# Kernel optimization log

Hardware: AMD Instinct MI355X
Metric: run time of the kernel (lower is better)

## Reference

```python
import jax, jax.numpy as jnp
import numpy as np

N, D_IN, E, H, F, T = 50000, 128, 800000, 8, 32, 8
NEG_SLOPE = 0.2


def setup_inputs() -> dict:
    key = jax.random.key(0)
    ks = jax.random.split(key, 12)
    feat = jax.random.normal(ks[0], (N, D_IN), dtype=jnp.float32)
    edge_embeddings = jax.random.normal(ks[1], (E, H), dtype=jnp.float32)
    src = jax.random.randint(ks[2], (E,), 0, N, dtype=jnp.int32)
    dst = jnp.sort(jax.random.randint(ks[3], (E,), 0, N, dtype=jnp.int32))
    etype = jax.random.randint(ks[4], (E,), 0, T, dtype=jnp.int32)
    s = 0.05
    W_src = jax.random.normal(ks[5], (H * F, D_IN), dtype=jnp.float32) * s
    attn_l = jax.random.normal(ks[6], (1, H, F), dtype=jnp.float32) * s
    attn_r = jax.random.normal(ks[7], (1, H, F), dtype=jnp.float32) * s
    attn_e = jax.random.normal(ks[8], (1, H, F), dtype=jnp.float32) * s
    W_e = jax.random.normal(ks[9], (H * F, H), dtype=jnp.float32) * s
    type_emb = jax.random.normal(ks[10], (T, F), dtype=jnp.float32) * s
    k2 = jax.random.split(ks[11], 3)
    W_et = jax.random.normal(k2[0], (H * F, F), dtype=jnp.float32) * s
    attn_et = jax.random.normal(k2[1], (1, H, F), dtype=jnp.float32) * s
    bias = jnp.zeros((H * F,), dtype=jnp.float32)
    return dict(feat=feat, edge_embeddings=edge_embeddings, src=src, dst=dst,
                etype=etype, W_src=W_src, attn_l=attn_l, attn_r=attn_r,
                attn_e=attn_e, W_e=W_e, type_emb=type_emb, W_et=W_et,
                attn_et=attn_et, bias=bias)


def _leaky_relu(x):
    return jnp.where(x >= 0, x, NEG_SLOPE * x)


def reference(feat, edge_embeddings, src, dst, etype, W_src, attn_l, attn_r,
              attn_e, W_e, type_emb, W_et, attn_et, bias):
    n = feat.shape[0]
    # node transform (shared src/dst weights)
    fs = (feat @ W_src.T).reshape(n, H, F)           # [N,H,F]
    el = (fs * attn_l).sum(-1)                        # [N,H]
    er = (fs * attn_r).sum(-1)                        # [N,H]
    e = el[src] + er[dst]                             # [E,H] (u_add_v)
    # edge embedding attention term
    ee = (edge_embeddings @ W_e.T).reshape(-1, H, F)  # [E,H,F]
    e_score = (ee * attn_e).sum(-1)                   # [E,H]
    # edge type embedding attention term
    te = type_emb[etype]                              # [E,F]
    te = (te @ W_et.T).reshape(-1, H, F)              # [E,H,F]
    t_score = (te * attn_et).sum(-1)                  # [E,H]
    attn = e + e_score + t_score                      # attn_agg = sum
    # edge-type frequency normalization
    counts = jnp.bincount(etype, length=T).astype(jnp.float32)
    w = counts.sum() / (T * counts)                   # [T]
    attn = attn * w[etype][:, None]
    attn = _leaky_relu(attn)                          # v2=False -> after agg
    # edge softmax over incoming edges of each dst node
    m = jax.ops.segment_max(attn, dst, num_segments=n)  # [N,H]
    a = jnp.exp(attn - m[dst])
    z = jax.ops.segment_sum(a, dst, num_segments=n)     # [N,H]
    a = a / z[dst]                                      # [E,H]
    # weighted scatter aggregation
    msg = fs[src] * a[:, :, None]                       # [E,H,F]
    out = jax.ops.segment_sum(msg, dst, num_segments=n) # [N,H,F]
    return out + bias.reshape(1, H, F)
```

## Files before the change

### kernel.cpp

```cpp
#include <hip/hip_runtime.h>
#include <math.h>

#define N_NODES 50000
#define D_IN    128
#define E_EDGES 800000
#define H_HEADS 8
#define F_FEAT  32
#define T_TYPES 8
#define HF      256
#define NEG_SLOPE 0.2f
#define HIST_BLOCKS 256
#define GEMM_BLOCKS 208
#define OFF_BLOCKS  196
#define K1_HIST_BASE GEMM_BLOCKS
#define K1_OFF_BASE  (GEMM_BLOCKS + HIST_BLOCKS)
#define K1_GRID      (GEMM_BLOCKS + HIST_BLOCKS + OFF_BLOCKS)
#define NGROUPS      ((N_NODES + 63) / 64)

using short8 = __attribute__((__ext_vector_type__(8))) short;
using f32x4  = __attribute__((__ext_vector_type__(4))) float;

__device__ inline float bf2f(unsigned short u) {
    union { unsigned int i; float f; } v; v.i = ((unsigned int)u) << 16; return v.f;
}
__device__ inline unsigned short f2bf(float f) {
    unsigned int x = __float_as_uint(f);
    unsigned int r = (x + 0x7fffu + ((x >> 16) & 1u)) >> 16;
    return (unsigned short)r;
}
__device__ inline unsigned int pk2bf(float a, float b) {
    return (unsigned int)f2bf(a) | ((unsigned int)f2bf(b) << 16);
}

__global__ __launch_bounds__(256) void prep_kernel(const float* __restrict__ feat,
                                                   const float* __restrict__ W,
                                                   const float* __restrict__ attn_l,
                                                   const float* __restrict__ attn_r,
                                                   const int*   __restrict__ etype,
                                                   const int*   __restrict__ dst,
                                                   unsigned short* __restrict__ fsb,
                                                   float* __restrict__ el,
                                                   float* __restrict__ er,
                                                   int* __restrict__ partials,
                                                   int* __restrict__ off) {
    __shared__ unsigned short Wl[HF * D_IN];
    __shared__ int sw[4][8];
    const int t = threadIdx.x;

    if (blockIdx.x >= K1_OFF_BASE) {
        int n = (blockIdx.x - K1_OFF_BASE) * 256 + t;
        if (n > N_NODES) return;
        int lo = 0, hi = E_EDGES;
        while (lo < hi) {
            int mid = (lo + hi) >> 1;
            if (dst[mid] < n) lo = mid + 1; else hi = mid;
        }
        off[n] = lo;
        return;
    }
    if (blockIdx.x >= K1_HIST_BASE) {
        const int hb = blockIdx.x - K1_HIST_BASE;
        int c[8] = {0,0,0,0,0,0,0,0};
        const int stride = HIST_BLOCKS * 256;
        for (int e = hb * 256 + t; e < E_EDGES; e += stride) {
            int ty = etype[e];
#pragma unroll
            for (int k = 0; k < 8; ++k) c[k] += (ty == k) ? 1 : 0;
        }
#pragma unroll
        for (int k = 0; k < 8; ++k) {
            c[k] += __shfl_xor(c[k], 1);  c[k] += __shfl_xor(c[k], 2);
            c[k] += __shfl_xor(c[k], 4);  c[k] += __shfl_xor(c[k], 8);
            c[k] += __shfl_xor(c[k], 16); c[k] += __shfl_xor(c[k], 32);
        }
        const int wv = t >> 6, l = t & 63;
        if (l == 0) {
#pragma unroll
            for (int k = 0; k < 8; ++k) sw[wv][k] = c[k];
        }
        __syncthreads();
        if (t < 8) partials[hb * 8 + t] = sw[0][t] + sw[1][t] + sw[2][t] + sw[3][t];
        return;
    }

    for (int i = 0; i < 16; ++i) {
        int slot = i * 256 + t;
        int n = slot >> 4, k16 = slot & 15;
        const float* wp = W + (size_t)n * D_IN + k16 * 8;
        float4 w0 = *(const float4*)wp;
        float4 w1 = *(const float4*)(wp + 4);
        union { unsigned int u[4]; short8 s; } ua;
        ua.u[0] = pk2bf(w0.x, w0.y); ua.u[1] = pk2bf(w0.z, w0.w);
        ua.u[2] = pk2bf(w1.x, w1.y); ua.u[3] = pk2bf(w1.z, w1.w);
        int idx = n * D_IN + ((k16 * 8) ^ ((n & 7) << 3));
        *(short8*)&Wl[idx] = ua.s;
    }
    __syncthreads();

    const int wid = t >> 6, l = t & 63;
    const int r16 = l & 15, kq = l >> 4;
    float alv0[8], alv1[8], arv0[8], arv1[8];
#pragma unroll
    for (int h = 0; h < 8; ++h) {
        alv0[h] = attn_l[h * 32 + r16];  alv1[h] = attn_l[h * 32 + 16 + r16];
        arv0[h] = attn_r[h * 32 + r16];  arv1[h] = attn_r[h * 32 + 16 + r16];
    }

    for (int grp = blockIdx.x; grp < NGROUPS; grp += GEMM_BLOCKS) {
        const int node0 = grp * 64 + wid * 16;
        int arow = node0 + r16;
        if (arow >= N_NODES) arow = N_NODES - 1;
        const float* fp = feat + (size_t)arow * D_IN + kq * 8;

        f32x4 acc[16];
#pragma unroll
        for (int i = 0; i < 16; ++i) acc[i] = (f32x4){0.f, 0.f, 0.f, 0.f};

#pragma unroll
        for (int kc = 0; kc < 4; ++kc) {
            float4 a0 = *(const float4*)(fp + kc * 32);
            float4 a1 = *(const float4*)(fp + kc * 32 + 4);
            union { unsigned int u[4]; short8 s; } ua;
            ua.u[0] = pk2bf(a0.x, a0.y); ua.u[1] = pk2bf(a0.z, a0.w);
            ua.u[2] = pk2bf(a1.x, a1.y); ua.u[3] = pk2bf(a1.z, a1.w);
            short8 af = ua.s;
#pragma unroll
            for (int nsub = 0; nsub < 16; ++nsub) {
                int n = nsub * 16 + r16;
                int idx = n * D_IN + ((kc * 32 + kq * 8) ^ ((n & 7) << 3));
                short8 bf = *(short8*)&Wl[idx];
                acc[nsub] = __builtin_amdgcn_mfma_f32_16x16x32_bf16(af, bf, acc[nsub], 0, 0, 0);
            }
        }

        const int nodeb = node0 + kq * 4;
#pragma unroll
        for (int h = 0; h < 8; ++h) {
            float ev[4], rv[4];
#pragma unroll
            for (int g = 0; g < 4; ++g) {
                ev[g] = acc[2 * h][g] * alv0[h] + acc[2 * h + 1][g] * alv1[h];
                rv[g] = acc[2 * h][g] * arv0[h] + acc[2 * h + 1][g] * arv1[h];
            }
#pragma unroll
            for (int g = 0; g < 4; ++g) {
                ev[g] += __shfl_xor(ev[g], 1); ev[g] += __shfl_xor(ev[g], 2);
                ev[g] += __shfl_xor(ev[g], 4); ev[g] += __shfl_xor(ev[g], 8);
                rv[g] += __shfl_xor(rv[g], 1); rv[g] += __shfl_xor(rv[g], 2);
                rv[g] += __shfl_xor(rv[g], 4); rv[g] += __shfl_xor(rv[g], 8);
            }
            if (r16 == 0) {
#pragma unroll
                for (int g = 0; g < 4; ++g) {
                    int nd = nodeb + g;
                    if (nd < N_NODES) {
                        el[nd * 8 + h] = ev[g];
                        er[nd * 8 + h] = rv[g];
                    }
                }
            }
        }
#pragma unroll
        for (int nsub = 0; nsub < 16; ++nsub) {
            int col = nsub * 16 + r16;
#pragma unroll
            for (int g = 0; g < 4; ++g) {
                int nd = nodeb + g;
                if (nd < N_NODES) fsb[(size_t)nd * HF + col] = f2bf(acc[nsub][g]);
            }
        }
    }
}

__global__ __launch_bounds__(256) void tables_kernel(const float* __restrict__ attn_e,
                              const float* __restrict__ W_e,
                              const float* __restrict__ attn_et,
                              const float* __restrict__ W_et,
                              const float* __restrict__ type_emb,
                              const int* __restrict__ partials,
                              float* __restrict__ M, float* __restrict__ ttab,
                              float* __restrict__ w) {
    __shared__ float q[8][32];
    int t = threadIdx.x;
    {
        int h = t >> 5, f2 = t & 31;
        float s = 0.f;
#pragma unroll 8
        for (int f = 0; f < F_FEAT; ++f)
            s += attn_et[h * 32 + f] * W_et[(h * 32 + f) * 32 + f2];
        q[h][f2] = s;
    }
    __syncthreads();
    if (t < 64) {
        int h = t >> 3, j = t & 7;
        float m = 0.f;
#pragma unroll 8
        for (int f = 0; f < F_FEAT; ++f)
            m += attn_e[h * 32 + f] * W_e[(h * 32 + f) * 8 + j];
        M[h * 8 + j] = m;
        float tt = 0.f;
#pragma unroll 8
        for (int f2 = 0; f2 < F_FEAT; ++f2)
            tt += type_emb[j * 32 + f2] * q[h][f2];
        ttab[j * 8 + h] = tt;
    }
    if (t < 64) {
        int j = t & 7, chunk = t >> 3;
        int c = 0;
#pragma unroll 8
        for (int b = 0; b < HIST_BLOCKS / 8; ++b)
            c += partials[(chunk * (HIST_BLOCKS / 8) + b) * 8 + j];
        c += __shfl_xor(c, 8); c += __shfl_xor(c, 16); c += __shfl_xor(c, 32);
        if (t < 8) {
            if (c < 1) c = 1;
            w[t] = (float)E_EDGES / (8.0f * (float)c);
        }
    }
}

__global__ __launch_bounds__(256) void edge_kernel(const float* __restrict__ ee,
        const int* __restrict__ src, const int* __restrict__ dst,
        const int* __restrict__ etype, const float* __restrict__ el,
        const float* __restrict__ er, const float* __restrict__ M,
        const float* __restrict__ ttab, const float* __restrict__ w,
        unsigned short* __restrict__ pexp) {
    __shared__ float sM[64], sT[64], sw[8];
    int t = threadIdx.x;
    if (t < 64) { sM[t] = M[t]; sT[t] = ttab[t]; }
    if (t < 8) sw[t] = w[t];
    __syncthreads();
    int e = blockIdx.x * 256 + t;
    if (e >= E_EDGES) return;
    int s = src[e], d = dst[e], ty = etype[e];
    float4 e0 = *(const float4*)&ee[(size_t)e * 8];
    float4 e1 = *(const float4*)&ee[(size_t)e * 8 + 4];
    float4 l0 = *(const float4*)&el[s * 8];
    float4 l1 = *(const float4*)&el[s * 8 + 4];
    float4 r0 = *(const float4*)&er[d * 8];
    float4 r1 = *(const float4*)&er[d * 8 + 4];
    float wt = sw[ty];
    float lv[8] = {l0.x,l0.y,l0.z,l0.w,l1.x,l1.y,l1.z,l1.w};
    float rv[8] = {r0.x,r0.y,r0.z,r0.w,r1.x,r1.y,r1.z,r1.w};
    unsigned int o[4];
#pragma unroll
    for (int hp = 0; hp < 4; ++hp) {
        float p2[2];
#pragma unroll
        for (int i = 0; i < 2; ++i) {
            int h = hp * 2 + i;
            float sc = lv[h] + rv[h] + sT[ty * 8 + h];
            sc += e0.x*sM[h*8+0] + e0.y*sM[h*8+1] + e0.z*sM[h*8+2] + e0.w*sM[h*8+3]
                + e1.x*sM[h*8+4] + e1.y*sM[h*8+5] + e1.z*sM[h*8+6] + e1.w*sM[h*8+7];
            sc *= wt;
            sc = (sc >= 0.f) ? sc : NEG_SLOPE * sc;
            p2[i] = __expf(sc);
        }
        o[hp] = (unsigned int)f2bf(p2[0]) | ((unsigned int)f2bf(p2[1]) << 16);
    }
    *(uint4*)&pexp[(size_t)e * 8] = make_uint4(o[0], o[1], o[2], o[3]);
}

__global__ __launch_bounds__(256) void agg_kernel(const unsigned short* __restrict__ pexp,
        const unsigned short* __restrict__ fsb, const int* __restrict__ src,
        const int* __restrict__ off, const float* __restrict__ bias,
        float* __restrict__ out) {
    const int wid = threadIdx.x >> 6;
    const int l = threadIdx.x & 63;
    const int n = blockIdx.x * 4 + wid;
    if (n >= N_NODES) return;
    const int beg = off[n], end = off[n + 1];
    const int c0 = 4 * l;
    const int h = l >> 3;
    const float4 b4 = *(const float4*)&bias[c0];
    float* op = &out[(size_t)n * HF + c0];
    if (beg == end) { *(float4*)op = b4; return; }
    float a0 = 0.f, a1 = 0.f, a2 = 0.f, a3 = 0.f, z = 0.f;
    for (int base = beg; base < end; base += 64) {
        const int remn = end - base;
        const int rem = remn < 64 ? remn : 64;
        int idx = base + l; if (idx >= end) idx = end - 1;
        const int sl = src[idx];
        int j = 0;
        for (; j + 8 <= rem; j += 8) {
            int   ss[8]; float pp[8]; ushort4 ff[8];
#pragma unroll
            for (int u = 0; u < 8; ++u) ss[u] = __shfl(sl, j + u);
#pragma unroll
            for (int u = 0; u < 8; ++u)
                pp[u] = bf2f(pexp[(size_t)(base + j + u) * 8 + h]);
#pragma unroll
            for (int u = 0; u < 8; ++u)
                ff[u] = *(const ushort4*)&fsb[(size_t)ss[u] * HF + c0];
#pragma unroll
            for (int u = 0; u < 8; ++u) {
                a0 += pp[u] * bf2f(ff[u].x); a1 += pp[u] * bf2f(ff[u].y);
                a2 += pp[u] * bf2f(ff[u].z); a3 += pp[u] * bf2f(ff[u].w);
                z += pp[u];
            }
        }
        for (; j < rem; ++j) {
            const int s0 = __shfl(sl, j);
            const float p0 = bf2f(pexp[(size_t)(base + j) * 8 + h]);
            const ushort4 f0 = *(const ushort4*)&fsb[(size_t)s0 * HF + c0];
            a0 += p0 * bf2f(f0.x); a1 += p0 * bf2f(f0.y);
            a2 += p0 * bf2f(f0.z); a3 += p0 * bf2f(f0.w); z += p0;
        }
    }
    const float rz = 1.f / z;
    *(float4*)op = make_float4(a0 * rz + b4.x, a1 * rz + b4.y,
                               a2 * rz + b4.z, a3 * rz + b4.w);
}

extern "C" void kernel_launch(void* const* d_in, const int* in_sizes, int n_in,
                              void* d_out, int out_size, void* d_ws, size_t ws_size,
                              hipStream_t stream) {
    const float* feat     = (const float*)d_in[0];
    const float* ee       = (const float*)d_in[1];
    const int*   src      = (const int*)d_in[2];
    const int*   dst      = (const int*)d_in[3];
    const int*   etype    = (const int*)d_in[4];
    const float* W_src    = (const float*)d_in[5];
    const float* attn_l   = (const float*)d_in[6];
    const float* attn_r   = (const float*)d_in[7];
    const float* attn_e   = (const float*)d_in[8];
    const float* W_e      = (const float*)d_in[9];
    const float* type_emb = (const float*)d_in[10];
    const float* W_et     = (const float*)d_in[11];
    const float* attn_et  = (const float*)d_in[12];
    const float* bias     = (const float*)d_in[13];
    float* out = (float*)d_out;

    char* ws = (char*)d_ws;
    size_t o = 0;
    auto alloc = [&](size_t bytes) -> void* {
        void* p = ws + o;
        o = (o + bytes + 255) & ~(size_t)255;
        return p;
    };
    unsigned short* fsb  = (unsigned short*)alloc((size_t)N_NODES * HF * 2);
    unsigned short* pexp = (unsigned short*)alloc((size_t)E_EDGES * 8 * 2);
    float* el    = (float*)alloc((size_t)N_NODES * 8 * 4);
    float* er    = (float*)alloc((size_t)N_NODES * 8 * 4);
    int*   off   = (int*)alloc((size_t)(N_NODES + 1) * 4);
    int*   partials = (int*)alloc((size_t)HIST_BLOCKS * 8 * 4);
    float* M     = (float*)alloc(64 * 4);
    float* ttab  = (float*)alloc(64 * 4);
    float* w     = (float*)alloc(T_TYPES * 4);

    prep_kernel<<<K1_GRID, 256, 0, stream>>>(feat, W_src, attn_l, attn_r,
                                             etype, dst, fsb, el, er,
                                             partials, off);
    tables_kernel<<<1, 256, 0, stream>>>(attn_e, W_e, attn_et, W_et, type_emb,
                                         partials, M, ttab, w);
    edge_kernel<<<(E_EDGES + 255) / 256, 256, 0, stream>>>(
        ee, src, dst, etype, el, er, M, ttab, w, pexp);
    agg_kernel<<<(N_NODES + 3) / 4, 256, 0, stream>>>(pexp, fsb, src, off, bias, out);
}
```

Before: 128.6 us.

## Fuse edge score computation into aggregation kernel via per-wave LDS staging

Removes the separate edge kernel. Each wave of the aggregation kernel now computes the leaky-ReLU attention exponentials for its 64-edge chunk, stages them as bf16 in shared memory and reads them back per head. The dst-side er term is loaded once per node instead of once per edge. This drops the global pexp buffer write and re-read plus one kernel launch. In exchange it adds edge-score arithmetic and the ee/el loads inside the latency-bound gather loop, and it cuts the inner unroll from 8 to 4, which may reduce memory-level parallelism.

```diff
diff --git a/kernel.cpp b/kernel.cpp
--- a/kernel.cpp
+++ b/kernel.cpp
@@ -218,89 +218,88 @@
     }
 }
 
-__global__ __launch_bounds__(256) void edge_kernel(const float* __restrict__ ee,
-        const int* __restrict__ src, const int* __restrict__ dst,
-        const int* __restrict__ etype, const float* __restrict__ el,
-        const float* __restrict__ er, const float* __restrict__ M,
-        const float* __restrict__ ttab, const float* __restrict__ w,
-        unsigned short* __restrict__ pexp) {
+__global__ __launch_bounds__(256) void agg_kernel(const float* __restrict__ ee,
+        const int* __restrict__ src, const int* __restrict__ etype,
+        const unsigned short* __restrict__ fsb, const float* __restrict__ el,
+        const float* __restrict__ er, const int* __restrict__ off,
+        const float* __restrict__ Mt, const float* __restrict__ ttab,
+        const float* __restrict__ w, const float* __restrict__ bias,
+        float* __restrict__ out) {
     __shared__ float sM[64], sT[64], sw[8];
-    int t = threadIdx.x;
-    if (t < 64) { sM[t] = M[t]; sT[t] = ttab[t]; }
-    if (t < 8) sw[t] = w[t];
+    __shared__ unsigned short plds[4][64][8];
+    const int t = threadIdx.x;
+    if (t < 64) { sM[t] = Mt[t]; sT[t] = ttab[t]; }
+    if (t >= 64 && t < 72) sw[t - 64] = w[t - 64];
     __syncthreads();
-    int e = blockIdx.x * 256 + t;
-    if (e >= E_EDGES) return;
-    int s = src[e], d = dst[e], ty = etype[e];
-    float4 e0 = *(const float4*)&ee[(size_t)e * 8];
-    float4 e1 = *(const float4*)&ee[(size_t)e * 8 + 4];
-    float4 l0 = *(const float4*)&el[s * 8];
-    float4 l1 = *(const float4*)&el[s * 8 + 4];
-    float4 r0 = *(const float4*)&er[d * 8];
-    float4 r1 = *(const float4*)&er[d * 8 + 4];
-    float wt = sw[ty];
-    float lv[8] = {l0.x,l0.y,l0.z,l0.w,l1.x,l1.y,l1.z,l1.w};
-    float rv[8] = {r0.x,r0.y,r0.z,r0.w,r1.x,r1.y,r1.z,r1.w};
-    unsigned int o[4];
-#pragma unroll
-    for (int hp = 0; hp < 4; ++hp) {
-        float p2[2];
-#pragma unroll
-        for (int i = 0; i < 2; ++i) {
-            int h = hp * 2 + i;
-            float sc = lv[h] + rv[h] + sT[ty * 8 + h];
-            sc += e0.x*sM[h*8+0] + e0.y*sM[h*8+1] + e0.z*sM[h*8+2] + e0.w*sM[h*8+3]
-                + e1.x*sM[h*8+4] + e1.y*sM[h*8+5] + e1.z*sM[h*8+6] + e1.w*sM[h*8+7];
-            sc *= wt;
-            sc = (sc >= 0.f) ? sc : NEG_SLOPE * sc;
-            p2[i] = __expf(sc);
-        }
-        o[hp] = (unsigned int)f2bf(p2[0]) | ((unsigned int)f2bf(p2[1]) << 16);
-    }
-    *(uint4*)&pexp[(size_t)e * 8] = make_uint4(o[0], o[1], o[2], o[3]);
-}
-
-__global__ __launch_bounds__(256) void agg_kernel(const unsigned short* __restrict__ pexp,
-        const unsigned short* __restrict__ fsb, const int* __restrict__ src,
-        const int* __restrict__ off, const float* __restrict__ bias,
-        float* __restrict__ out) {
-    const int wid = threadIdx.x >> 6;
-    const int l = threadIdx.x & 63;
+    const int wid = t >> 6, l = t & 63;
     const int n = blockIdx.x * 4 + wid;
     if (n >= N_NODES) return;
     const int beg = off[n], end = off[n + 1];
-    const int c0 = 4 * l;
-    const int h = l >> 3;
+    const int c0 = 4 * l, h = l >> 3;
     const float4 b4 = *(const float4*)&bias[c0];
     float* op = &out[(size_t)n * HF + c0];
     if (beg == end) { *(float4*)op = b4; return; }
+    const float4 r0v = *(const float4*)&er[n * 8];
+    const float4 r1v = *(const float4*)&er[n * 8 + 4];
+    const float rv[8] = {r0v.x,r0v.y,r0v.z,r0v.w,r1v.x,r1v.y,r1v.z,r1v.w};
+    unsigned short* myp = &plds[wid][0][0];
     float a0 = 0.f, a1 = 0.f, a2 = 0.f, a3 = 0.f, z = 0.f;
     for (int base = beg; base < end; base += 64) {
         const int remn = end - base;
         const int rem = remn < 64 ? remn : 64;
         int idx = base + l; if (idx >= end) idx = end - 1;
         const int sl = src[idx];
+        const int ty = etype[idx];
+        {
+            const float* eep = &ee[(size_t)idx * 8];
+            const float4 e0 = *(const float4*)eep;
+            const float4 e1 = *(const float4*)(eep + 4);
+            const float4 l0 = *(const float4*)&el[sl * 8];
+            const float4 l1 = *(const float4*)&el[sl * 8 + 4];
+            const float wt = sw[ty];
+            const float lv[8] = {l0.x,l0.y,l0.z,l0.w,l1.x,l1.y,l1.z,l1.w};
+            unsigned int o[4];
+#pragma unroll
+            for (int hp = 0; hp < 4; ++hp) {
+                float p2[2];
+#pragma unroll
+                for (int i = 0; i < 2; ++i) {
+                    int hh = hp * 2 + i;
+                    float sc = lv[hh] + rv[hh] + sT[ty * 8 + hh];
+                    sc += e0.x*sM[hh*8+0] + e0.y*sM[hh*8+1] + e0.z*sM[hh*8+2] + e0.w*sM[hh*8+3]
+                        + e1.x*sM[hh*8+4] + e1.y*sM[hh*8+5] + e1.z*sM[hh*8+6] + e1.w*sM[hh*8+7];
+                    sc *= wt;
+                    sc = (sc >= 0.f) ? sc : NEG_SLOPE * sc;
+                    p2[i] = __expf(sc);
+                }
+                o[hp] = pk2bf(p2[0], p2[1]);
+            }
+            *(uint4*)&myp[l * 8] = make_uint4(o[0], o[1], o[2], o[3]);
+        }
         int j = 0;
-        for (; j + 8 <= rem; j += 8) {
-            int   ss[8]; float pp[8]; ushort4 ff[8];
-#pragma unroll
-            for (int u = 0; u < 8; ++u) ss[u] = __shfl(sl, j + u);
-#pragma unroll
-            for (int u = 0; u < 8; ++u)
-                pp[u] = bf2f(pexp[(size_t)(base + j + u) * 8 + h]);
-#pragma unroll
-            for (int u = 0; u < 8; ++u)
-                ff[u] = *(const ushort4*)&fsb[(size_t)ss[u] * HF + c0];
-#pragma unroll
-            for (int u = 0; u < 8; ++u) {
-                a0 += pp[u] * bf2f(ff[u].x); a1 += pp[u] * bf2f(ff[u].y);
-                a2 += pp[u] * bf2f(ff[u].z); a3 += pp[u] * bf2f(ff[u].w);
-                z += pp[u];
-            }
+        for (; j + 4 <= rem; j += 4) {
+            const int s0 = __shfl(sl, j),     s1 = __shfl(sl, j + 1);
+            const int s2 = __shfl(sl, j + 2), s3 = __shfl(sl, j + 3);
+            const float p0 = bf2f(myp[(j    ) * 8 + h]);
+            const float p1 = bf2f(myp[(j + 1) * 8 + h]);
+            const float p2 = bf2f(myp[(j + 2) * 8 + h]);
+            const float p3 = bf2f(myp[(j + 3) * 8 + h]);
+            const ushort4 f0 = *(const ushort4*)&fsb[(size_t)s0 * HF + c0];
+            const ushort4 f1 = *(const ushort4*)&fsb[(size_t)s1 * HF + c0];
+            const ushort4 f2 = *(const ushort4*)&fsb[(size_t)s2 * HF + c0];
+            const ushort4 f3 = *(const ushort4*)&fsb[(size_t)s3 * HF + c0];
+            a0 += p0 * bf2f(f0.x); a1 += p0 * bf2f(f0.y);
+            a2 += p0 * bf2f(f0.z); a3 += p0 * bf2f(f0.w); z += p0;
+            a0 += p1 * bf2f(f1.x); a1 += p1 * bf2f(f1.y);
+            a2 += p1 * bf2f(f1.z); a3 += p1 * bf2f(f1.w); z += p1;
+            a0 += p2 * bf2f(f2.x); a1 += p2 * bf2f(f2.y);
+            a2 += p2 * bf2f(f2.z); a3 += p2 * bf2f(f2.w); z += p2;
+            a0 += p3 * bf2f(f3.x); a1 += p3 * bf2f(f3.y);
+            a2 += p3 * bf2f(f3.z); a3 += p3 * bf2f(f3.w); z += p3;
         }
         for (; j < rem; ++j) {
             const int s0 = __shfl(sl, j);
-            const float p0 = bf2f(pexp[(size_t)(base + j) * 8 + h]);
+            const float p0 = bf2f(myp[j * 8 + h]);
             const ushort4 f0 = *(const ushort4*)&fsb[(size_t)s0 * HF + c0];
             a0 += p0 * bf2f(f0.x); a1 += p0 * bf2f(f0.y);
             a2 += p0 * bf2f(f0.z); a3 += p0 * bf2f(f0.w); z += p0;
@@ -338,7 +337,6 @@
         return p;
     };
     unsigned short* fsb  = (unsigned short*)alloc((size_t)N_NODES * HF * 2);
-    unsigned short* pexp = (unsigned short*)alloc((size_t)E_EDGES * 8 * 2);
     float* el    = (float*)alloc((size_t)N_NODES * 8 * 4);
     float* er    = (float*)alloc((size_t)N_NODES * 8 * 4);
     int*   off   = (int*)alloc((size_t)(N_NODES + 1) * 4);
@@ -352,7 +350,6 @@
                                              partials, off);
     tables_kernel<<<1, 256, 0, stream>>>(attn_e, W_e, attn_et, W_et, type_emb,
                                          partials, M, ttab, w);
-    edge_kernel<<<(E_EDGES + 255) / 256, 256, 0, stream>>>(
-        ee, src, dst, etype, el, er, M, ttab, w, pexp);
-    agg_kernel<<<(N_NODES + 3) / 4, 256, 0, stream>>>(pexp, fsb, src, off, bias, out);
-}
+    agg_kernel<<<(N_NODES + 3) / 4, 256, 0, stream>>>(ee, src, etype, fsb, el, er,
+                                                      off, M, ttab, w, bias, out);
+}
```

Measured after the change: 177.3 us. +37.9%, slower.
